# Kernel tuning notes

Measured on AMD Instinct MI355X. Metric: run time of the kernel, lower is better.

## Reference

```python
import jax, jax.numpy as jnp
import numpy as np

N_HEADS = 8
TOPK = 64
LN_EPS = 1e-5


def layernorm(x, g, b):
    mu = jnp.mean(x, axis=-1, keepdims=True)
    var = jnp.mean((x - mu) ** 2, axis=-1, keepdims=True)
    return (x - mu) * jax.lax.rsqrt(var + LN_EPS) * g + b


def mha(x, wq, wk, wv, wo, causal):
    # x: [B, S, H]; weights are torch nn.Linear style [out, in]
    B, S, H = x.shape
    hd = H // N_HEADS
    scale = 1.0 / np.sqrt(hd)

    def proj(w):
        return (x @ w.T).reshape(B, S, N_HEADS, hd).transpose(0, 2, 1, 3)  # [B, n, S, hd]

    q, k, v = proj(wq), proj(wk), proj(wv)
    s = jnp.einsum('bnqd,bnkd->bnqk', q, k) * scale
    if causal:
        m = jnp.tril(jnp.ones((S, S), bool))
        s = jnp.where(m, s, jnp.finfo(s.dtype).min)
    a = jax.nn.softmax(s, axis=-1)
    o = jnp.einsum('bnqk,bnkd->bnqd', a, v).transpose(0, 2, 1, 3).reshape(B, S, H)
    return o @ wo.T


def topk_activation(x, k):
    # x: [N, F]; keep top-k per row, zero elsewhere (matches topk + scatter_)
    vals, idx = jax.lax.top_k(x, k)
    rows = jnp.arange(x.shape[0])[:, None]
    return jnp.zeros_like(x).at[rows, idx].set(vals)


def setup_inputs() -> dict:
    key = jax.random.key(0)
    B, D, L, H, F = 8, 16, 128, 512, 4096
    ks = jax.random.split(key, 12)
    s = 1.0 / np.sqrt(H)
    w = lambda k, shp, sc: jax.random.normal(k, shp, jnp.float32) * sc
    return {
        'zL': w(ks[0], (B, D, L, H), 1.0),
        'wq_l': w(ks[1], (H, H), s), 'wk_l': w(ks[2], (H, H), s),
        'wv_l': w(ks[3], (H, H), s), 'wo_l': w(ks[4], (H, H), s),
        'gamma_l': jnp.ones(H, jnp.float32), 'beta_l': jnp.zeros(H, jnp.float32),
        'wq_d': w(ks[5], (H, H), s), 'wk_d': w(ks[6], (H, H), s),
        'wv_d': w(ks[7], (H, H), s), 'wo_d': w(ks[8], (H, H), s),
        'gamma_d': jnp.ones(H, jnp.float32), 'beta_d': jnp.zeros(H, jnp.float32),
        'dict_enc': w(ks[9], (F, H), np.sqrt(2.0 / (H + F))),
        'bias_pre': jnp.zeros(H, jnp.float32),
        'bias_enc': jnp.zeros(F, jnp.float32),
        'query_token': jnp.zeros(H, jnp.float32),
    }


def reference(zL, wq_l, wk_l, wv_l, wo_l, gamma_l, beta_l,
              wq_d, wk_d, wv_d, wo_d, gamma_d, beta_d,
              dict_enc, bias_pre, bias_enc, query_token):
    B, D, L, H = zL.shape
    F = dict_enc.shape[0]
    # prepend learned query token along depth, drop last layer
    qt = jnp.broadcast_to(query_token[None, None, None, :], (B, 1, L, H))
    x = jnp.concatenate([qt, zL[:, :-1, :, :]], axis=1)  # [B, D, L, H]
    # non-causal attention over L within each (b, d)
    x = x.reshape(B * D, L, H)
    x = x + mha(layernorm(x, gamma_l, beta_l), wq_l, wk_l, wv_l, wo_l, causal=False)
    # causal attention over D within each (b, l)
    x = x.reshape(B, D, L, H).transpose(0, 2, 1, 3).reshape(B * L, D, H)
    x = x + mha(layernorm(x, gamma_d, beta_d), wq_d, wk_d, wv_d, wo_d, causal=True)
    x_prior = x.reshape(B, L, D, H).transpose(0, 2, 1, 3)  # [B, D, L, H]
    # dictionary encode on residual (detached in original)
    N = B * D * L
    x_src = jax.lax.stop_gradient(zL - x_prior).reshape(N, H)
    logits = (x_src - bias_pre[None, :]) @ dict_enc.T + bias_enc
    z_dense = jax.nn.relu(logits)
    z_flat = topk_activation(z_dense, TOPK)
    z_n = z_flat.reshape(B, D, L, F)
    return z_n, x_prior
```

## Files before the change

### kernel.cpp

```cpp
#include <hip/hip_runtime.h>
#include <stdint.h>

#define NTOK 16384
#define HDIM 512
#define FDIM 4096
#define NHEAD 8

typedef __attribute__((ext_vector_type(8))) _Float16 f16x8;
typedef __attribute__((ext_vector_type(16))) float f32x16;
#define LOSCALE 4096.0f
#define LOINV   (1.0f / 4096.0f)

static __device__ __forceinline__ void ld8f(const float* p, float* v) {
    *(float4*)&v[0] = *(const float4*)p;
    *(float4*)&v[4] = *(const float4*)(p + 4);
}
static __device__ __forceinline__ void st8f(float* p, const float* v) {
    *(float4*)p       = *(const float4*)&v[0];
    *(float4*)(p + 4) = *(const float4*)&v[4];
}

__global__ __launch_bounds__(256) void build_x_k(const float* __restrict__ zL,
                                                 const float* __restrict__ qt,
                                                 float* __restrict__ X) {
    int idx = blockIdx.x * 256 + threadIdx.x;
    int n = idx >> 6;
    int h = (idx & 63) << 3;
    int d = (n >> 7) & 15;
    const float* src = d ? (zL + (((size_t)(n - 128)) << 9) + h) : (qt + h);
    float v[8];
    ld8f(src, v);
    st8f(X + (((size_t)n) << 9) + h, v);
}

__global__ __launch_bounds__(256) void ln_split_k(const float* __restrict__ X,
                                                  const float* __restrict__ gamma,
                                                  const float* __restrict__ beta,
                                                  _Float16* __restrict__ ph,
                                                  _Float16* __restrict__ pl) {
    int row = blockIdx.x * 4 + (threadIdx.x >> 6);
    int lane = threadIdx.x & 63;
    int h = lane << 3;
    const float* xr = X + (((size_t)row) << 9) + h;
    float v[8];
    ld8f(xr, v);
    float s = 0.f;
#pragma unroll
    for (int i = 0; i < 8; ++i) s += v[i];
#pragma unroll
    for (int off = 32; off; off >>= 1) s += __shfl_xor(s, off);
    float m = s * (1.0f / 512.0f);
    float q = 0.f;
#pragma unroll
    for (int i = 0; i < 8; ++i) { float d = v[i] - m; q += d * d; }
#pragma unroll
    for (int off = 32; off; off >>= 1) q += __shfl_xor(q, off);
    float rs = 1.0f / sqrtf(q * (1.0f / 512.0f) + 1e-5f);
    float gv[8], be[8];
    ld8f(gamma + h, gv);
    ld8f(beta + h, be);
    _Float16 h8[8], l8[8];
#pragma unroll
    for (int i = 0; i < 8; ++i) {
        float y = (v[i] - m) * rs * gv[i] + be[i];
        _Float16 hh = (_Float16)y;
        h8[i] = hh;
        l8[i] = (_Float16)((y - (float)hh) * LOSCALE);
    }
    size_t off = (((size_t)row) << 9) + h;
    *(int4*)(ph + off) = *(int4*)h8;
    *(int4*)(pl + off) = *(int4*)l8;
}

__global__ __launch_bounds__(512) void attn_l_k(const float* __restrict__ Q,
                                                const float* __restrict__ K,
                                                const float* __restrict__ V,
                                                _Float16* __restrict__ xh,
                                                _Float16* __restrict__ xl) {
    __shared__ float ks[128][64];
    __shared__ float vs[128][64];
    const int seq = blockIdx.x, head = blockIdx.y;
    const int t = threadIdx.x;
    const size_t base = (((size_t)seq) << 16) + (head << 6);
#pragma unroll
    for (int i = 0; i < 4; ++i) {
        int slot = t + (i << 9);
        int row = slot >> 4;
        int c4 = (slot & 15) << 2;
        size_t g = base + (((size_t)row) << 9) + c4;
        *(float4*)&ks[row][c4] = *(const float4*)(K + g);
        *(float4*)&vs[row][c4] = *(const float4*)(V + g);
    }
    __syncthreads();
    const int r = t >> 2;
    const int q16 = (t & 3) << 4;
    const float* qp = Q + base + (((size_t)r) << 9) + q16;
    float qr[16];
#pragma unroll
    for (int i = 0; i < 4; ++i) *(float4*)&qr[i << 2] = *(const float4*)(qp + (i << 2));
    float o[16];
#pragma unroll
    for (int d = 0; d < 16; ++d) o[d] = 0.f;
    float m = -1e30f, l = 0.f;
    for (int j = 0; j < 128; ++j) {
        const float* kp = &ks[j][q16];
        float s0 = 0.f, s1 = 0.f, s2 = 0.f, s3 = 0.f;
#pragma unroll
        for (int d = 0; d < 16; d += 4) {
            s0 = fmaf(qr[d + 0], kp[d + 0], s0);
            s1 = fmaf(qr[d + 1], kp[d + 1], s1);
            s2 = fmaf(qr[d + 2], kp[d + 2], s2);
            s3 = fmaf(qr[d + 3], kp[d + 3], s3);
        }
        float sp = (s0 + s1) + (s2 + s3);
        sp += __shfl_xor(sp, 1);
        sp += __shfl_xor(sp, 2);
        float s = sp * 0.125f;
        if (s > m) {
            float c = expf(m - s);
#pragma unroll
            for (int d = 0; d < 16; ++d) o[d] *= c;
            l *= c;
            m = s;
        }
        float w = expf(s - m);
        l += w;
        const float* vp = &vs[j][q16];
#pragma unroll
        for (int d = 0; d < 16; ++d) o[d] = fmaf(w, vp[d], o[d]);
    }
    float inv = 1.0f / l;
    _Float16 h8[16], l8[16];
#pragma unroll
    for (int i = 0; i < 16; ++i) {
        float y = o[i] * inv;
        _Float16 hh = (_Float16)y;
        h8[i] = hh;
        l8[i] = (_Float16)((y - (float)hh) * LOSCALE);
    }
    size_t eo = base + (((size_t)r) << 9) + q16;
    *(int4*)(xh + eo)     = ((int4*)h8)[0];
    *(int4*)(xh + eo + 8) = ((int4*)h8)[1];
    *(int4*)(xl + eo)     = ((int4*)l8)[0];
    *(int4*)(xl + eo + 8) = ((int4*)l8)[1];
}

__global__ __launch_bounds__(128) void attn_d_k(const float* __restrict__ Q,
                                                const float* __restrict__ K,
                                                const float* __restrict__ V,
                                                _Float16* __restrict__ xh,
                                                _Float16* __restrict__ xl) {
    __shared__ float ks[16][512];
    __shared__ float vs[16][512];
    const int bl = blockIdx.x;
    const int b = bl >> 7, l = bl & 127;
    const int t = threadIdx.x;
    const size_t base = ((size_t)(b * 2048 + l)) << 9;
#pragma unroll
    for (int i = 0; i < 16; ++i) {
        int slot = t + (i << 7);
        int row = slot >> 7;
        int c4 = (slot & 127) << 2;
        size_t g = base + (((size_t)row) << 16) + c4;
        *(float4*)&ks[row][c4] = *(const float4*)(K + g);
        *(float4*)&vs[row][c4] = *(const float4*)(V + g);
    }
    __syncthreads();
    const int head = t >> 4, dr = t & 15;
    const int ho = head << 6;
    float qr[64];
    const float* qp = Q + base + (((size_t)dr) << 16) + ho;
#pragma unroll
    for (int i = 0; i < 16; ++i) *(float4*)&qr[i << 2] = *(const float4*)(qp + (i << 2));
    float s[16];
    float m = -1e30f;
#pragma unroll
    for (int j = 0; j < 16; ++j) {
        float s0 = 0.f, s1 = 0.f, s2 = 0.f, s3 = 0.f;
#pragma unroll
        for (int d = 0; d < 64; d += 4) {
            s0 = fmaf(qr[d + 0], ks[j][ho + d + 0], s0);
            s1 = fmaf(qr[d + 1], ks[j][ho + d + 1], s1);
            s2 = fmaf(qr[d + 2], ks[j][ho + d + 2], s2);
            s3 = fmaf(qr[d + 3], ks[j][ho + d + 3], s3);
        }
        float sv = ((s0 + s1) + (s2 + s3)) * 0.125f;
        s[j] = (j <= dr) ? sv : -1e30f;
        m = fmaxf(m, s[j]);
    }
    float lsum = 0.f;
#pragma unroll
    for (int j = 0; j < 16; ++j) {
        float w = (j <= dr) ? expf(s[j] - m) : 0.f;
        s[j] = w;
        lsum += w;
    }
    float inv = 1.0f / lsum;
    float o[64];
#pragma unroll
    for (int d = 0; d < 64; ++d) o[d] = 0.f;
#pragma unroll
    for (int j = 0; j < 16; ++j) {
        float w = s[j];
#pragma unroll
        for (int d = 0; d < 64; ++d) o[d] = fmaf(w, vs[j][ho + d], o[d]);
    }
    size_t eo = base + (((size_t)dr) << 16) + ho;
#pragma unroll
    for (int i = 0; i < 8; ++i) {
        _Float16 h8[8], l8[8];
#pragma unroll
        for (int j = 0; j < 8; ++j) {
            float y = o[i * 8 + j] * inv;
            _Float16 hh = (_Float16)y;
            h8[j] = hh;
            l8[j] = (_Float16)((y - (float)hh) * LOSCALE);
        }
        *(int4*)(xh + eo + (i << 3)) = *(int4*)h8;
        *(int4*)(xl + eo + (i << 3)) = *(int4*)l8;
    }
}

__global__ __launch_bounds__(256) void xprior_xsrc_k(const float* __restrict__ zL,
                                                     const float* __restrict__ bias_pre,
                                                     const float* __restrict__ X,
                                                     float* __restrict__ out_xp,
                                                     _Float16* __restrict__ xh,
                                                     _Float16* __restrict__ xl) {
    int idx = blockIdx.x * 256 + threadIdx.x;
    int h = (idx & 63) << 3;
    size_t off = ((size_t)idx) << 3;
    float z[8], p[8], x[8];
    ld8f(zL + off, z);
    ld8f(bias_pre + h, p);
    ld8f(X + off, x);
    st8f(out_xp + off, x);
    _Float16 h8[8], l8[8];
#pragma unroll
    for (int i = 0; i < 8; ++i) {
        float y = z[i] - x[i] - p[i];
        _Float16 hh = (_Float16)y;
        h8[i] = hh;
        l8[i] = (_Float16)((y - (float)hh) * LOSCALE);
    }
    *(int4*)(xh + off) = *(int4*)h8;
    *(int4*)(xl + off) = *(int4*)l8;
}

__global__ __launch_bounds__(256) void split2_k(const float* __restrict__ in,
                                                _Float16* __restrict__ ph,
                                                _Float16* __restrict__ pl) {
    int idx = blockIdx.x * 256 + threadIdx.x;
    float v[8];
    ld8f(in + (((size_t)idx) << 3), v);
    _Float16 h8[8], l8[8];
#pragma unroll
    for (int i = 0; i < 8; ++i) {
        _Float16 h = (_Float16)v[i];
        float r = v[i] - (float)h;
        h8[i] = h;
        l8[i] = (_Float16)(r * LOSCALE);
    }
    *(int4*)(ph + (((size_t)idx) << 3)) = *(int4*)h8;
    *(int4*)(pl + (((size_t)idx) << 3)) = *(int4*)l8;
}

#define LDT 34
template<bool ADD_C, bool BIAS>
__global__ __launch_bounds__(256) void gemm_f16_k(
        const _Float16* __restrict__ Xh, const _Float16* __restrict__ Xl,
        const _Float16* __restrict__ Wh, const _Float16* __restrict__ Wl,
        const float* __restrict__ bias, float* __restrict__ Cout, int ldc) {
    __shared__ _Float16 Ah[2][128][LDT], Al[2][128][LDT];
    __shared__ _Float16 Bh[2][64][LDT],  Bl[2][64][LDT];
    const int tid = threadIdx.x;
    const int bm = blockIdx.y << 7;
    const int bn = blockIdx.x << 6;
    const int w = tid >> 6, lane = tid & 63;
    const int wr = w >> 1, wc = w & 1;
    const int l31 = lane & 31, hh = lane >> 5;
    const int ar0 = tid >> 2, akg = (tid & 3) << 3;
    const int ar1 = ar0 + 64;
    const _Float16* pXh0 = Xh + (size_t)(bm + ar0) * HDIM + akg;
    const _Float16* pXl0 = Xl + (size_t)(bm + ar0) * HDIM + akg;
    const _Float16* pXh1 = Xh + (size_t)(bm + ar1) * HDIM + akg;
    const _Float16* pXl1 = Xl + (size_t)(bm + ar1) * HDIM + akg;
    const _Float16* pWh  = Wh + (size_t)(bn + ar0) * HDIM + akg;
    const _Float16* pWl  = Wl + (size_t)(bn + ar0) * HDIM + akg;

    f32x16 acc1[2], acc2[2];
#pragma unroll
    for (int i = 0; i < 2; ++i)
#pragma unroll
        for (int r = 0; r < 16; ++r) { acc1[i][r] = 0.f; acc2[i][r] = 0.f; }

    int4 ra0h, ra0l, ra1h, ra1l, rbh, rbl;
    auto LOADR = [&](int k0) {
        ra0h = *(const int4*)(pXh0 + k0);
        ra0l = *(const int4*)(pXl0 + k0);
        ra1h = *(const int4*)(pXh1 + k0);
        ra1l = *(const int4*)(pXl1 + k0);
        rbh  = *(const int4*)(pWh + k0);
        rbl  = *(const int4*)(pWl + k0);
    };
    auto STORE = [&](int buf) {
        *(int4*)&Ah[buf][ar0][akg] = ra0h;
        *(int4*)&Al[buf][ar0][akg] = ra0l;
        *(int4*)&Ah[buf][ar1][akg] = ra1h;
        *(int4*)&Al[buf][ar1][akg] = ra1l;
        *(int4*)&Bh[buf][ar0][akg] = rbh;
        *(int4*)&Bl[buf][ar0][akg] = rbl;
    };

    LOADR(0);
    STORE(0);
    int cur = 0;
    for (int it = 0; it < 16; ++it) {
        if (it < 15) LOADR((it + 1) << 5);
        __syncthreads();
#pragma unroll
        for (int kh = 0; kh < 2; ++kh) {
            const int ko = (kh << 4) + (hh << 3);
            f16x8 fah[2], fal[2];
#pragma unroll
            for (int mf = 0; mf < 2; ++mf) {
                int ar = (wr << 6) + (mf << 5) + l31;
                fah[mf] = *(const f16x8*)&Ah[cur][ar][ko];
                fal[mf] = *(const f16x8*)&Al[cur][ar][ko];
            }
            int bc_ = (wc << 5) + l31;
            f16x8 bh = *(const f16x8*)&Bh[cur][bc_][ko];
            f16x8 bl = *(const f16x8*)&Bl[cur][bc_][ko];
#pragma unroll
            for (int mf = 0; mf < 2; ++mf) {
                acc1[mf] = __builtin_amdgcn_mfma_f32_32x32x16_f16(fah[mf], bh, acc1[mf], 0, 0, 0);
                acc2[mf] = __builtin_amdgcn_mfma_f32_32x32x16_f16(fah[mf], bl, acc2[mf], 0, 0, 0);
                acc2[mf] = __builtin_amdgcn_mfma_f32_32x32x16_f16(fal[mf], bh, acc2[mf], 0, 0, 0);
            }
        }
        if (it < 15) { STORE(cur ^ 1); cur ^= 1; }
    }
    const int col = bn + (wc << 5) + l31;
    const float badd = BIAS ? bias[col] : 0.f;
#pragma unroll
    for (int mf = 0; mf < 2; ++mf) {
#pragma unroll
        for (int r = 0; r < 16; ++r) {
            int row = bm + (wr << 6) + (mf << 5) + (r & 3) + ((r >> 2) << 3) + (hh << 2);
            float* cp = Cout + (size_t)row * ldc + col;
            float val = acc1[mf][r] + acc2[mf][r] * LOINV + badd;
            if (ADD_C) val += *cp;
            *cp = val;
        }
    }
}

__global__ __launch_bounds__(256) void topk_k(const float* __restrict__ logits,
                                              float* __restrict__ out) {
    const int row = blockIdx.x;
    const float* lr = logits + (((size_t)row) << 12);
    const int t = threadIdx.x;
    float v[16]; uint32_t u[16];
#pragma unroll
    for (int i = 0; i < 16; ++i) {
        float x = fmaxf(lr[t + (i << 8)], 0.f);
        v[i] = x;
        u[i] = __float_as_uint(x);
    }
    __shared__ int red[4];
    __shared__ unsigned long long bits[64];
    __shared__ int s_cut;
    uint32_t prefix = 0;
    bool exact = false;
    for (int bit = 30; bit >= 0; --bit) {
        uint32_t c = prefix | (1u << bit);
        int cnt = 0;
#pragma unroll
        for (int i = 0; i < 16; ++i) cnt += (u[i] >= c) ? 1 : 0;
#pragma unroll
        for (int off = 32; off; off >>= 1) cnt += __shfl_xor(cnt, off);
        if ((t & 63) == 0) red[t >> 6] = cnt;
        __syncthreads();
        int total = red[0] + red[1] + red[2] + red[3];
        __syncthreads();
        if (total >= 64) prefix = c;
        if (total == 64) { exact = true; break; }
    }
    float* orow = out + (((size_t)row) << 12);
    if (exact) {
#pragma unroll
        for (int i = 0; i < 16; ++i) {
            int col = t + (i << 8);
            orow[col] = (u[i] >= prefix) ? v[i] : 0.f;
        }
        return;
    }
    const uint32_t T64 = prefix;
    int cg = 0;
#pragma unroll
    for (int i = 0; i < 16; ++i) cg += (u[i] > T64) ? 1 : 0;
#pragma unroll
    for (int off = 32; off; off >>= 1) cg += __shfl_xor(cg, off);
    if ((t & 63) == 0) red[t >> 6] = cg;
    __syncthreads();
    const int ngt = red[0] + red[1] + red[2] + red[3];
    int cut = -1;
    if (T64 != 0u) {
        const int r = 64 - ngt;
        if (t < 64) bits[t] = 0ull;
        __syncthreads();
#pragma unroll
        for (int i = 0; i < 16; ++i) {
            if (u[i] == T64) {
                int col = t + (i << 8);
                atomicOr(&bits[col >> 6], 1ull << (col & 63));
            }
        }
        __syncthreads();
        if (t == 0) {
            int need = r, cs = FDIM - 1;
            for (int wd = 0; wd < 64; ++wd) {
                int pc = __popcll(bits[wd]);
                if (need <= pc) {
                    unsigned long long bb = bits[wd];
                    for (int q = 1; q < need; ++q) bb &= bb - 1;
                    cs = (wd << 6) + (__ffsll(bb) - 1);
                    break;
                }
                need -= pc;
            }
            s_cut = cs;
        }
        __syncthreads();
        cut = s_cut;
    }
#pragma unroll
    for (int i = 0; i < 16; ++i) {
        int col = t + (i << 8);
        bool keep = (u[i] > T64) || (T64 != 0u && u[i] == T64 && col <= cut);
        orow[col] = keep ? v[i] : 0.f;
    }
}

extern "C" void kernel_launch(void* const* d_in, const int* in_sizes, int n_in,
                              void* d_out, int out_size, void* d_ws, size_t ws_size,
                              hipStream_t stream) {
    const float* zL      = (const float*)d_in[0];
    const float* gamma_l = (const float*)d_in[5];
    const float* beta_l  = (const float*)d_in[6];
    const float* gamma_d = (const float*)d_in[11];
    const float* beta_d  = (const float*)d_in[12];
    const float* dict_e  = (const float*)d_in[13];
    const float* bias_pre= (const float*)d_in[14];
    const float* bias_enc= (const float*)d_in[15];
    const float* qt      = (const float*)d_in[16];
    const float* wproj[8] = { (const float*)d_in[1], (const float*)d_in[2],
                              (const float*)d_in[3], (const float*)d_in[4],
                              (const float*)d_in[7], (const float*)d_in[8],
                              (const float*)d_in[9], (const float*)d_in[10] };

    float* out_z  = (float*)d_out;
    float* out_xp = out_z + (size_t)NTOK * FDIM;

    const size_t NHf = (size_t)NTOK * HDIM;
    float* B0 = (float*)d_out;
    float* B1 = B0 + NHf;
    float* B2 = B1 + NHf;
    float* B3 = B2 + NHf;

    float* wsf    = (float*)d_ws;
    float* logits = wsf + 64;

    const size_t dictE = (size_t)FDIM * HDIM;
    const size_t WE    = (size_t)HDIM * HDIM;

    int crows = NTOK;
    const size_t fixedB = 64 * sizeof(float)
                        + (2 * dictE + 16 * WE + 2 * NHf) * sizeof(_Float16);
    while (crows > 128 && fixedB + (size_t)crows * FDIM * sizeof(float) > ws_size)
        crows >>= 1;

    _Float16* dh = (_Float16*)(logits + (size_t)crows * FDIM);
    _Float16* dl = dh + dictE;
    _Float16* wsp = dh + 2 * dictE;
    _Float16* xh = wsp + 16 * WE;
    _Float16* xl = xh + NHf;
    _Float16* wh[8], *wl[8];
    for (int i = 0; i < 8; ++i) {
        wh[i] = wsp + (size_t)i * 2 * WE;
        wl[i] = wh[i] + WE;
    }

    const dim3 blk256(256), blk128(128), blk512(512);
    const dim3 gElem(4096);
    const dim3 gProjM(HDIM / 64, NTOK / 128);

    for (int i = 0; i < 8; ++i)
        split2_k<<<dim3(WE / 8 / 256), blk256, 0, stream>>>(wproj[i], wh[i], wl[i]);
    split2_k<<<dim3(dictE / 8 / 256), blk256, 0, stream>>>(dict_e, dh, dl);

    build_x_k<<<gElem, blk256, 0, stream>>>(zL, qt, B0);

    ln_split_k<<<dim3(NTOK / 4), blk256, 0, stream>>>(B0, gamma_l, beta_l, xh, xl);
    gemm_f16_k<false, false><<<gProjM, blk256, 0, stream>>>(xh, xl, wh[0], wl[0], nullptr, B1, HDIM);
    gemm_f16_k<false, false><<<gProjM, blk256, 0, stream>>>(xh, xl, wh[1], wl[1], nullptr, B2, HDIM);
    gemm_f16_k<false, false><<<gProjM, blk256, 0, stream>>>(xh, xl, wh[2], wl[2], nullptr, B3, HDIM);
    attn_l_k<<<dim3(128, NHEAD), blk512, 0, stream>>>(B1, B2, B3, xh, xl);
    gemm_f16_k<true, false><<<gProjM, blk256, 0, stream>>>(xh, xl, wh[3], wl[3], nullptr, B0, HDIM);

    ln_split_k<<<dim3(NTOK / 4), blk256, 0, stream>>>(B0, gamma_d, beta_d, xh, xl);
    gemm_f16_k<false, false><<<gProjM, blk256, 0, stream>>>(xh, xl, wh[4], wl[4], nullptr, B1, HDIM);
    gemm_f16_k<false, false><<<gProjM, blk256, 0, stream>>>(xh, xl, wh[5], wl[5], nullptr, B2, HDIM);
    gemm_f16_k<false, false><<<gProjM, blk256, 0, stream>>>(xh, xl, wh[6], wl[6], nullptr, B3, HDIM);
    attn_d_k<<<dim3(1024), blk128, 0, stream>>>(B1, B2, B3, xh, xl);
    gemm_f16_k<true, false><<<gProjM, blk256, 0, stream>>>(xh, xl, wh[7], wl[7], nullptr, B0, HDIM);

    xprior_xsrc_k<<<gElem, blk256, 0, stream>>>(zL, bias_pre, B0, out_xp, xh, xl);

    const dim3 gDict(FDIM / 64, crows / 128);
    for (int c0 = 0; c0 < NTOK; c0 += crows) {
        gemm_f16_k<false, true><<<gDict, blk256, 0, stream>>>(
            xh + (size_t)c0 * HDIM, xl + (size_t)c0 * HDIM,
            dh, dl, bias_enc, logits, FDIM);
        topk_k<<<dim3(crows), blk256, 0, stream>>>(logits, out_z + (size_t)c0 * FDIM);
    }
}
```

Baseline: 1.176 ms.

## Fuse Q/K/V projections into one GEMM with interleaved QKV output

Stacks the Q, K and V weight splits contiguously so a single GEMM with output width 1536 produces an interleaved QKV buffer. Both attention kernels now read Q, K and V from that strided buffer. This cuts two GEMM launches per attention layer and reads the split activations once instead of three times, at the cost of strided loads in the attention kernels. It also caps dictionary chunk rows at 2048, which shrinks the logits workspace but adds more chunked GEMM and top-k launches.

```diff
diff --git a/kernel.cpp b/kernel.cpp
--- a/kernel.cpp
+++ b/kernel.cpp
@@ -5,6 +5,7 @@
 #define HDIM 512
 #define FDIM 4096
 #define NHEAD 8
+#define QKVD 1536
 
 typedef __attribute__((ext_vector_type(8))) _Float16 f16x8;
 typedef __attribute__((ext_vector_type(16))) float f32x16;
@@ -72,29 +73,28 @@
     *(int4*)(pl + off) = *(int4*)l8;
 }
 
-__global__ __launch_bounds__(512) void attn_l_k(const float* __restrict__ Q,
-                                                const float* __restrict__ K,
-                                                const float* __restrict__ V,
+__global__ __launch_bounds__(512) void attn_l_k(const float* __restrict__ QKV,
                                                 _Float16* __restrict__ xh,
                                                 _Float16* __restrict__ xl) {
     __shared__ float ks[128][64];
     __shared__ float vs[128][64];
     const int seq = blockIdx.x, head = blockIdx.y;
     const int t = threadIdx.x;
-    const size_t base = (((size_t)seq) << 16) + (head << 6);
+    const size_t tok0 = (size_t)seq << 7;
+    const int ho = head << 6;
 #pragma unroll
     for (int i = 0; i < 4; ++i) {
         int slot = t + (i << 9);
         int row = slot >> 4;
         int c4 = (slot & 15) << 2;
-        size_t g = base + (((size_t)row) << 9) + c4;
-        *(float4*)&ks[row][c4] = *(const float4*)(K + g);
-        *(float4*)&vs[row][c4] = *(const float4*)(V + g);
+        size_t g = (tok0 + row) * QKVD + ho + c4;
+        *(float4*)&ks[row][c4] = *(const float4*)(QKV + g + 512);
+        *(float4*)&vs[row][c4] = *(const float4*)(QKV + g + 1024);
     }
     __syncthreads();
     const int r = t >> 2;
     const int q16 = (t & 3) << 4;
-    const float* qp = Q + base + (((size_t)r) << 9) + q16;
+    const float* qp = QKV + (tok0 + r) * QKVD + ho + q16;
     float qr[16];
 #pragma unroll
     for (int i = 0; i < 4; ++i) *(float4*)&qr[i << 2] = *(const float4*)(qp + (i << 2));
@@ -138,16 +138,14 @@
         h8[i] = hh;
         l8[i] = (_Float16)((y - (float)hh) * LOSCALE);
     }
-    size_t eo = base + (((size_t)r) << 9) + q16;
+    size_t eo = ((tok0 + r) << 9) + ho + q16;
     *(int4*)(xh + eo)     = ((int4*)h8)[0];
     *(int4*)(xh + eo + 8) = ((int4*)h8)[1];
     *(int4*)(xl + eo)     = ((int4*)l8)[0];
     *(int4*)(xl + eo + 8) = ((int4*)l8)[1];
 }
 
-__global__ __launch_bounds__(128) void attn_d_k(const float* __restrict__ Q,
-                                                const float* __restrict__ K,
-                                                const float* __restrict__ V,
+__global__ __launch_bounds__(128) void attn_d_k(const float* __restrict__ QKV,
                                                 _Float16* __restrict__ xh,
                                                 _Float16* __restrict__ xl) {
     __shared__ float ks[16][512];
@@ -155,21 +153,19 @@
     const int bl = blockIdx.x;
     const int b = bl >> 7, l = bl & 127;
     const int t = threadIdx.x;
-    const size_t base = ((size_t)(b * 2048 + l)) << 9;
+    const size_t tok0 = (size_t)b * 2048 + l;
 #pragma unroll
     for (int i = 0; i < 16; ++i) {
-        int slot = t + (i << 7);
-        int row = slot >> 7;
-        int c4 = (slot & 127) << 2;
-        size_t g = base + (((size_t)row) << 16) + c4;
-        *(float4*)&ks[row][c4] = *(const float4*)(K + g);
-        *(float4*)&vs[row][c4] = *(const float4*)(V + g);
+        int c4 = t << 2;
+        size_t g = (tok0 + (size_t)i * 128) * QKVD + c4;
+        *(float4*)&ks[i][c4] = *(const float4*)(QKV + g + 512);
+        *(float4*)&vs[i][c4] = *(const float4*)(QKV + g + 1024);
     }
     __syncthreads();
     const int head = t >> 4, dr = t & 15;
     const int ho = head << 6;
     float qr[64];
-    const float* qp = Q + base + (((size_t)dr) << 16) + ho;
+    const float* qp = QKV + (tok0 + (size_t)dr * 128) * QKVD + ho;
 #pragma unroll
     for (int i = 0; i < 16; ++i) *(float4*)&qr[i << 2] = *(const float4*)(qp + (i << 2));
     float s[16];
@@ -205,7 +201,7 @@
 #pragma unroll
         for (int d = 0; d < 64; ++d) o[d] = fmaf(w, vs[j][ho + d], o[d]);
     }
-    size_t eo = base + (((size_t)dr) << 16) + ho;
+    size_t eo = ((tok0 + (size_t)dr * 128) << 9) + ho;
 #pragma unroll
     for (int i = 0; i < 8; ++i) {
         _Float16 h8[8], l8[8];
@@ -465,8 +461,6 @@
     const size_t NHf = (size_t)NTOK * HDIM;
     float* B0 = (float*)d_out;
     float* B1 = B0 + NHf;
-    float* B2 = B1 + NHf;
-    float* B3 = B2 + NHf;
 
     float* wsf    = (float*)d_ws;
     float* logits = wsf + 64;
@@ -474,46 +468,53 @@
     const size_t dictE = (size_t)FDIM * HDIM;
     const size_t WE    = (size_t)HDIM * HDIM;
 
-    int crows = NTOK;
+    int crows = 2048;
     const size_t fixedB = 64 * sizeof(float)
                         + (2 * dictE + 16 * WE + 2 * NHf) * sizeof(_Float16);
     while (crows > 128 && fixedB + (size_t)crows * FDIM * sizeof(float) > ws_size)
         crows >>= 1;
 
-    _Float16* dh = (_Float16*)(logits + (size_t)crows * FDIM);
-    _Float16* dl = dh + dictE;
+    _Float16* dh  = (_Float16*)(logits + (size_t)crows * FDIM);
+    _Float16* dl  = dh + dictE;
     _Float16* wsp = dh + 2 * dictE;
-    _Float16* xh = wsp + 16 * WE;
-    _Float16* xl = xh + NHf;
-    _Float16* wh[8], *wl[8];
-    for (int i = 0; i < 8; ++i) {
-        wh[i] = wsp + (size_t)i * 2 * WE;
-        wl[i] = wh[i] + WE;
-    }
+    _Float16* xh  = wsp + 16 * WE;
+    _Float16* xl  = xh + NHf;
+    _Float16* qkvh_l = wsp;
+    _Float16* qkvl_l = wsp + 3 * WE;
+    _Float16* woh_l  = wsp + 6 * WE;
+    _Float16* wol_l  = wsp + 7 * WE;
+    _Float16* qkvh_d = wsp + 8 * WE;
+    _Float16* qkvl_d = wsp + 11 * WE;
+    _Float16* woh_d  = wsp + 14 * WE;
+    _Float16* wol_d  = wsp + 15 * WE;
 
     const dim3 blk256(256), blk128(128), blk512(512);
     const dim3 gElem(4096);
-    const dim3 gProjM(HDIM / 64, NTOK / 128);
-
-    for (int i = 0; i < 8; ++i)
-        split2_k<<<dim3(WE / 8 / 256), blk256, 0, stream>>>(wproj[i], wh[i], wl[i]);
+    const dim3 gW(WE / 8 / 256);
+    const dim3 gQKV(QKVD / 64, NTOK / 128);
+    const dim3 gWo(HDIM / 64, NTOK / 128);
+
+    split2_k<<<gW, blk256, 0, stream>>>(wproj[0], qkvh_l,          qkvl_l);
+    split2_k<<<gW, blk256, 0, stream>>>(wproj[1], qkvh_l + WE,     qkvl_l + WE);
+    split2_k<<<gW, blk256, 0, stream>>>(wproj[2], qkvh_l + 2 * WE, qkvl_l + 2 * WE);
+    split2_k<<<gW, blk256, 0, stream>>>(wproj[3], woh_l,           wol_l);
+    split2_k<<<gW, blk256, 0, stream>>>(wproj[4], qkvh_d,          qkvl_d);
+    split2_k<<<gW, blk256, 0, stream>>>(wproj[5], qkvh_d + WE,     qkvl_d + WE);
+    split2_k<<<gW, blk256, 0, stream>>>(wproj[6], qkvh_d + 2 * WE, qkvl_d + 2 * WE);
+    split2_k<<<gW, blk256, 0, stream>>>(wproj[7], woh_d,           wol_d);
     split2_k<<<dim3(dictE / 8 / 256), blk256, 0, stream>>>(dict_e, dh, dl);
 
     build_x_k<<<gElem, blk256, 0, stream>>>(zL, qt, B0);
 
     ln_split_k<<<dim3(NTOK / 4), blk256, 0, stream>>>(B0, gamma_l, beta_l, xh, xl);
-    gemm_f16_k<false, false><<<gProjM, blk256, 0, stream>>>(xh, xl, wh[0], wl[0], nullptr, B1, HDIM);
-    gemm_f16_k<false, false><<<gProjM, blk256, 0, stream>>>(xh, xl, wh[1], wl[1], nullptr, B2, HDIM);
-    gemm_f16_k<false, false><<<gProjM, blk256, 0, stream>>>(xh, xl, wh[2], wl[2], nullptr, B3, HDIM);
-    attn_l_k<<<dim3(128, NHEAD), blk512, 0, stream>>>(B1, B2, B3, xh, xl);
-    gemm_f16_k<true, false><<<gProjM, blk256, 0, stream>>>(xh, xl, wh[3], wl[3], nullptr, B0, HDIM);
+    gemm_f16_k<false, false><<<gQKV, blk256, 0, stream>>>(xh, xl, qkvh_l, qkvl_l, nullptr, B1, QKVD);
+    attn_l_k<<<dim3(128, NHEAD), blk512, 0, stream>>>(B1, xh, xl);
+    gemm_f16_k<true, false><<<gWo, blk256, 0, stream>>>(xh, xl, woh_l, wol_l, nullptr, B0, HDIM);
 
     ln_split_k<<<dim3(NTOK / 4), blk256, 0, stream>>>(B0, gamma_d, beta_d, xh, xl);
-    gemm_f16_k<false, false><<<gProjM, blk256, 0, stream>>>(xh, xl, wh[4], wl[4], nullptr, B1, HDIM);
-    gemm_f16_k<false, false><<<gProjM, blk256, 0, stream>>>(xh, xl, wh[5], wl[5], nullptr, B2, HDIM);
-    gemm_f16_k<false, false><<<gProjM, blk256, 0, stream>>>(xh, xl, wh[6], wl[6], nullptr, B3, HDIM);
-    attn_d_k<<<dim3(1024), blk128, 0, stream>>>(B1, B2, B3, xh, xl);
-    gemm_f16_k<true, false><<<gProjM, blk256, 0, stream>>>(xh, xl, wh[7], wl[7], nullptr, B0, HDIM);
+    gemm_f16_k<false, false><<<gQKV, blk256, 0, stream>>>(xh, xl, qkvh_d, qkvl_d, nullptr, B1, QKVD);
+    attn_d_k<<<dim3(1024), blk128, 0, stream>>>(B1, xh, xl);
+    gemm_f16_k<true, false><<<gWo, blk256, 0, stream>>>(xh, xl, woh_d, wol_d, nullptr, B0, HDIM);
 
     xprior_xsrc_k<<<gElem, blk256, 0, stream>>>(zL, bias_pre, B0, out_xp, xh, xl);
 
```

Result: no change. 1.192 ms (+1.3%).
